# Kernel tuning notes

Measured on AMD Instinct MI355X. Metric: run time of the kernel, lower is better.

Reference implementation:

```python
import jax, jax.numpy as jnp
import numpy as np

B = 64
LMAX = 1024
LENS = np.where(np.arange(B) % 2 == 0, 512, 1024)  # total 49152 residues
NP = int(LENS.sum())
NC_PER = 40
NC = B * NC_PER
DEG_C = 4
DEG_P = 8


def setup_inputs() -> dict:
    key = jax.random.key(0)
    ks = jax.random.split(key, 40)
    rng = np.random.default_rng(0)

    # ragged packing gather: row i of padded conv output contributes its first LENS[i] rows
    prot_gather = jnp.asarray(
        np.concatenate([i * LMAX + np.arange(l) for i, l in enumerate(LENS)]), jnp.int32)
    protein_batch = jnp.asarray(np.repeat(np.arange(B), LENS), jnp.int32)
    compound_batch = jnp.asarray(np.repeat(np.arange(B), NC_PER), jnp.int32)

    # protein edges: within-graph random contacts, DEG_P per residue
    p_starts = np.concatenate([[0], np.cumsum(LENS)])[:-1]
    src, tgt = [], []
    for i, l in enumerate(LENS):
        e = DEG_P * int(l)
        src.append(p_starts[i] + rng.integers(0, l, e))
        tgt.append(p_starts[i] + rng.integers(0, l, e))
    prot_src = jnp.asarray(np.concatenate(src), jnp.int32)
    prot_tgt = jnp.asarray(np.concatenate(tgt), jnp.int32)

    # compound edges: within-graph, DEG_C per atom
    gc = np.repeat(np.arange(B), NC_PER * DEG_C) * NC_PER
    comp_src = jnp.asarray(gc + rng.integers(0, NC_PER, B * NC_PER * DEG_C), jnp.int32)
    comp_tgt = jnp.asarray(gc + rng.integers(0, NC_PER, B * NC_PER * DEG_C), jnp.int32)

    n = lambda k, s: jax.random.normal(ks[k], s, jnp.float32) * 0.05
    return {
        'seq_x': jax.random.normal(ks[0], (B, LMAX, 21), jnp.float32),
        'compound_x': jax.random.normal(ks[1], (NC, 78), jnp.float32),
        'conv_w': n(2, (128, 21, 5)), 'conv_b': n(3, (128,)),
        'c1_wl': n(4, (78, 128)), 'c1_bl': n(5, (128,)), 'c1_wr': n(6, (78, 128)),
        'c2_wl': n(7, (128, 256)), 'c2_bl': n(8, (256,)), 'c2_wr': n(9, (128, 256)),
        'c3_wl': n(10, (256, 512)), 'c3_bl': n(11, (512,)), 'c3_wr': n(12, (256, 512)),
        'cfc_w': n(13, (512, 128)), 'cfc_b': n(14, (128,)),
        'p1_wl': n(15, (128, 128)), 'p1_bl': n(16, (128,)), 'p1_wr': n(17, (128, 128)),
        'p2_wl': n(18, (128, 256)), 'p2_bl': n(19, (256,)), 'p2_wr': n(20, (128, 256)),
        'p3_wl': n(21, (256, 512)), 'p3_bl': n(22, (512,)), 'p3_wr': n(23, (256, 512)),
        'pfc_w': n(24, (512, 128)), 'pfc_b': n(25, (128,)),
        'fc1_w': n(26, (256, 256)), 'fc1_b': n(27, (256,)),
        'out_w': n(28, (256, 1)), 'out_b': n(29, (1,)),
        'prot_gather': prot_gather, 'prot_src': prot_src, 'prot_tgt': prot_tgt,
        'comp_src': comp_src, 'comp_tgt': comp_tgt,
        'protein_batch': protein_batch, 'compound_batch': compound_batch,
    }


def _conv1d(x, w, b):
    # x: [B, L, Cin]; Conv1d(21->128, k=5, stride=1, pad=2)
    y = jax.lax.conv_general_dilated(x.transpose(0, 2, 1), w, (1,), [(2, 2)],
                                     dimension_numbers=('NCH', 'OIH', 'NCH'))
    return y.transpose(0, 2, 1) + b


def _sage(x, src, tgt, wl, bl, wr, n_nodes):
    # PyG SAGEConv(aggr='sum'): lin_l(sum_{j->i} x_j) + lin_r(x_i), lin_r has no bias
    agg = jax.ops.segment_sum(x[src], tgt, num_segments=n_nodes)
    return agg @ wl + bl + x @ wr


def reference(seq_x, compound_x, conv_w, conv_b,
              c1_wl, c1_bl, c1_wr, c2_wl, c2_bl, c2_wr, c3_wl, c3_bl, c3_wr,
              cfc_w, cfc_b,
              p1_wl, p1_bl, p1_wr, p2_wl, p2_bl, p2_wr, p3_wl, p3_bl, p3_wr,
              pfc_w, pfc_b, fc1_w, fc1_b, out_w, out_b,
              prot_gather, prot_src, prot_tgt, comp_src, comp_tgt,
              protein_batch, compound_batch):
    lrelu = jax.nn.leaky_relu  # slope 0.01 == nn.LeakyReLU default
    seq = _conv1d(seq_x, conv_w, conv_b)                 # [B, LMAX, 128]
    p = seq.reshape(-1, seq.shape[-1])[prot_gather]      # ragged pack -> [NP, 128]

    c = compound_x
    c = lrelu(_sage(c, comp_src, comp_tgt, c1_wl, c1_bl, c1_wr, NC))
    c = lrelu(_sage(c, comp_src, comp_tgt, c2_wl, c2_bl, c2_wr, NC))
    c = lrelu(_sage(c, comp_src, comp_tgt, c3_wl, c3_bl, c3_wr, NC))

    p = lrelu(_sage(p, prot_src, prot_tgt, p1_wl, p1_bl, p1_wr, NP))
    p = lrelu(_sage(p, prot_src, prot_tgt, p2_wl, p2_bl, p2_wr, NP))
    p = lrelu(_sage(p, prot_src, prot_tgt, p3_wl, p3_bl, p3_wr, NP))

    c = jax.ops.segment_max(c, compound_batch, num_segments=B)  # global max pool
    c = lrelu(c @ cfc_w + cfc_b)                                # dropout = identity (eval)
    p = jax.ops.segment_max(p, protein_batch, num_segments=B)
    p = lrelu(p @ pfc_w + pfc_b)

    x = jnp.concatenate([c, p], axis=1)
    x = lrelu(x @ fc1_w + fc1_b)
    return x @ out_w + out_b                                    # [B, 1]
```

## Files before the change

### kernel.cpp

```cpp
#include <hip/hip_runtime.h>
#include <hip/hip_fp16.h>

#define B_GRAPHS 64
#define LMAX 1024
#define NP_TOT 49152
#define NC_TOT 2560
#define EP_TOT 393216
#define EC_TOT 10240

#define SCAN_N   (NP_TOT + NC_TOT)
#define SCAN_BLK 512
#define SCAN_NB  (SCAN_N / SCAN_BLK)

typedef _Float16 f16x8 __attribute__((ext_vector_type(8)));
typedef _Float16 f16x4 __attribute__((ext_vector_type(4)));
typedef _Float16 f16x2 __attribute__((ext_vector_type(2)));
typedef float    f32x4 __attribute__((ext_vector_type(4)));

__device__ __forceinline__ float lrelu(float x) { return x > 0.f ? x : 0.01f * x; }

__global__ void zero_int_kernel(int* p, int n) {
    int i = blockIdx.x * blockDim.x + threadIdx.x;
    if (i < n) p[i] = 0;
}

__global__ void hist2_kernel(const int* __restrict__ ptgt, int* __restrict__ pdeg,
                             const int* __restrict__ ctgt, int* __restrict__ cdeg) {
    int e = blockIdx.x * blockDim.x + threadIdx.x;
    if (e < EP_TOT) atomicAdd(&pdeg[ptgt[e]], 1);
    else if (e < EP_TOT + EC_TOT) atomicAdd(&cdeg[ctgt[e - EP_TOT]], 1);
}

__global__ __launch_bounds__(256) void scan_bsum_kernel(
    const int* __restrict__ deg, int* __restrict__ bsums)
{
    __shared__ int red[256];
    int b = blockIdx.x, t = threadIdx.x;
    int2 e = *(const int2*)(deg + b * SCAN_BLK + t * 2);
    red[t] = e.x + e.y;
    __syncthreads();
    for (int s = 128; s > 0; s >>= 1) {
        if (t < s) red[t] += red[t + s];
        __syncthreads();
    }
    if (t == 0) bsums[b] = red[0];
}

__global__ __launch_bounds__(128) void scan_sums_kernel(int* __restrict__ bsums)
{
    __shared__ int v[SCAN_NB];
    int t = threadIdx.x;
    if (t < SCAN_NB) v[t] = bsums[t];
    __syncthreads();
    if (t == 0) {
        int run = 0;
        for (int i = 0; i < SCAN_NB; ++i) { int x = v[i]; v[i] = run; run += x; }
    }
    __syncthreads();
    if (t < SCAN_NB) bsums[t] = v[t];
}

__global__ __launch_bounds__(256) void scan_final_kernel(
    const int* __restrict__ deg, const int* __restrict__ bsums,
    int* __restrict__ p_rowptr, int* __restrict__ c_rowptr)
{
    __shared__ int wsum[4];
    int b = blockIdx.x, t = threadIdx.x;
    int i = b * SCAN_BLK + t * 2;
    int2 e = *(const int2*)(deg + i);
    int ts = e.x + e.y;
    int lane = t & 63, wv = t >> 6;
    int x = ts;
    #pragma unroll
    for (int o = 1; o < 64; o <<= 1) {
        int y = __shfl_up(x, o);
        if (lane >= o) x += y;
    }
    if (lane == 63) wsum[wv] = x;
    __syncthreads();
    int base = bsums[b];
    for (int w = 0; w < wv; ++w) base += wsum[w];
    int excl = base + x - ts;
    int v0 = excl, v1 = excl + e.x;
    if (i < NP_TOT) p_rowptr[i] = v0; else c_rowptr[i - NP_TOT] = v0 - EP_TOT;
    if (i + 1 < NP_TOT) p_rowptr[i + 1] = v1; else c_rowptr[i + 1 - NP_TOT] = v1 - EP_TOT;
    if (b == 0 && t == 0) { p_rowptr[NP_TOT] = EP_TOT; c_rowptr[NC_TOT] = EC_TOT; }
}

__global__ void scatter2_kernel(const int* __restrict__ ps, const int* __restrict__ pt,
                                const int* __restrict__ prow, int* __restrict__ pcur,
                                int* __restrict__ pcsr,
                                const int* __restrict__ cs, const int* __restrict__ ct,
                                const int* __restrict__ crow, int* __restrict__ ccur,
                                int* __restrict__ ccsr) {
    int e = blockIdx.x * blockDim.x + threadIdx.x;
    if (e < EP_TOT) {
        int t = pt[e];
        int pos = atomicAdd(&pcur[t], 1);
        pcsr[prow[t] + pos] = ps[e];
    } else if (e < EP_TOT + EC_TOT) {
        int e2 = e - EP_TOT;
        int t = ct[e2];
        int pos = atomicAdd(&ccur[t], 1);
        ccsr[crow[t] + pos] = cs[e2];
    }
}

struct WJob { const float* in; _Float16* out; int K, D, Kp, mode; };
struct WJobs { WJob j[13]; };

__global__ __launch_bounds__(256) void wprep_all_kernel(WJobs jobs) {
    WJob jb = jobs.j[blockIdx.z];
    int idx = blockIdx.x * 256 + threadIdx.x;
    int total = jb.D * jb.Kp;
    if (idx >= total) return;
    float v;
    if (jb.mode == 0) {
        int d = idx / jb.Kp, k = idx - d * jb.Kp;
        v = (k < jb.K) ? jb.in[(long)k * jb.D + d] : 0.f;
    } else {
        int o = idx >> 7, j = idx & 127;
        if (j < 105) {
            int k = j / 21, c = j - k * 21;
            v = jb.in[o * 105 + c * 5 + k];
        } else v = 0.f;
    }
    jb.out[idx] = (_Float16)v;
}

__global__ void cx_conv_kernel(const float* __restrict__ in, _Float16* __restrict__ out) {
    int i = blockIdx.x * 256 + threadIdx.x;
    if (i >= NC_TOT * 128) return;
    int r = i >> 7, k = i & 127;
    out[i] = (_Float16)(k < 78 ? in[r * 78 + k] : 0.f);
}

__global__ __launch_bounds__(256) void im2col_kernel(
    const float* __restrict__ seq, const int* __restrict__ gather,
    _Float16* __restrict__ out)
{
    int t4 = blockIdx.x * 256 + threadIdx.x;
    int i = t4 >> 5;
    if (i >= NP_TOT) return;
    int j0 = (t4 & 31) * 4;
    int g = gather[i];
    int bb = g >> 10, l = g & (LMAX - 1);
    f16x4 o;
    #pragma unroll
    for (int u = 0; u < 4; ++u) {
        int j = j0 + u;
        float v = 0.f;
        if (j < 105) {
            int k = j / 21, c = j - k * 21;
            int ll = l + k - 2;
            if ((unsigned)ll < (unsigned)LMAX)
                v = seq[((long)bb * LMAX + ll) * 21 + c];
        }
        o[u] = (_Float16)v;
    }
    *(f16x4*)(out + (long)i * 128 + j0) = o;
}

__global__ __launch_bounds__(256) void gemm_f16_kernel(
    const _Float16* __restrict__ A0, const _Float16* __restrict__ WT0,
    const _Float16* __restrict__ A1, const _Float16* __restrict__ WT1,
    const float* __restrict__ bias, _Float16* __restrict__ Out,
    int N, int K, int D, int npass, int act)
{
    __shared__ _Float16 Asm[128 * 64];
    __shared__ _Float16 Bsm[128 * 64];
    const int tid = threadIdx.x;
    const int wave = tid >> 6, lane = tid & 63;
    const int wr = wave >> 1, wc = wave & 1;
    const int l15 = lane & 15, lk = lane >> 4;
    const long r0 = (long)blockIdx.x * 128;
    const long c0 = (long)blockIdx.y * 128;

    const int srow = tid >> 1, shalf = tid & 1;
    int wofs[4];
    #pragma unroll
    for (int j = 0; j < 4; ++j) {
        int c = shalf * 4 + j;
        wofs[j] = srow * 64 + ((c ^ (srow & 7)) * 8);
    }

    int aoff[4][2], boff[4][2];
    #pragma unroll
    for (int m = 0; m < 4; ++m) {
        int row = wr * 64 + m * 16 + l15;
        int col = wc * 64 + m * 16 + l15;
        #pragma unroll
        for (int kk = 0; kk < 2; ++kk) {
            aoff[m][kk] = row * 64 + (((kk * 4 + lk) ^ (row & 7)) * 8);
            boff[m][kk] = col * 64 + (((kk * 4 + lk) ^ (col & 7)) * 8);
        }
    }

    f32x4 acc[4][4];
    #pragma unroll
    for (int m = 0; m < 4; ++m)
        #pragma unroll
        for (int n = 0; n < 4; ++n)
            #pragma unroll
            for (int i = 0; i < 4; ++i) acc[m][n][i] = 0.f;

    const int ksteps = K >> 6;
    const int S = ksteps * npass;

    f16x8 av[4], bv[4];
    #pragma unroll
    for (int j = 0; j < 4; ++j) {
        long kb = (long)(shalf * 4 + j) * 8;
        av[j] = *(const f16x8*)(A0  + (r0 + srow) * K + kb);
        bv[j] = *(const f16x8*)(WT0 + (c0 + srow) * K + kb);
    }

    for (int s = 0; s < S; ++s) {
        __syncthreads();
        #pragma unroll
        for (int j = 0; j < 4; ++j) *(f16x8*)(Asm + wofs[j]) = av[j];
        #pragma unroll
        for (int j = 0; j < 4; ++j) *(f16x8*)(Bsm + wofs[j]) = bv[j];
        __syncthreads();
        if (s + 1 < S) {
            int s1 = s + 1;
            int pass = (s1 >= ksteps) ? 1 : 0;
            long kb0 = (long)(s1 - pass * ksteps) * 64;
            const _Float16* Ax = pass ? A1 : A0;
            const _Float16* Wx = pass ? WT1 : WT0;
            #pragma unroll
            for (int j = 0; j < 4; ++j) {
                long kb = kb0 + (shalf * 4 + j) * 8;
                av[j] = *(const f16x8*)(Ax + (r0 + srow) * K + kb);
                bv[j] = *(const f16x8*)(Wx + (c0 + srow) * K + kb);
            }
        }
        #pragma unroll
        for (int kk = 0; kk < 2; ++kk) {
            f16x8 af[4], bf[4];
            #pragma unroll
            for (int m = 0; m < 4; ++m) af[m] = *(const f16x8*)(Asm + aoff[m][kk]);
            #pragma unroll
            for (int n = 0; n < 4; ++n) bf[n] = *(const f16x8*)(Bsm + boff[n][kk]);
            #pragma unroll
            for (int m = 0; m < 4; ++m)
                #pragma unroll
                for (int n = 0; n < 4; ++n)
                    acc[m][n] = __builtin_amdgcn_mfma_f32_16x16x32_f16(af[m], bf[n], acc[m][n], 0, 0, 0);
        }
    }

    float bn[4]; int coln[4];
    #pragma unroll
    for (int n = 0; n < 4; ++n) {
        coln[n] = (int)c0 + wc * 64 + n * 16 + l15;
        bn[n] = bias[coln[n]];
    }
    #pragma unroll
    for (int m = 0; m < 4; ++m) {
        long rowb = r0 + wr * 64 + m * 16 + lk * 4;
        #pragma unroll
        for (int i = 0; i < 4; ++i) {
            long row = rowb + i;
            #pragma unroll
            for (int n = 0; n < 4; ++n) {
                float v = acc[m][n][i] + bn[n];
                if (act) v = v > 0.f ? v : 0.01f * v;
                Out[row * D + coln[n]] = (_Float16)v;
            }
        }
    }
}

template<int D>
__global__ __launch_bounds__(256) void agg_f16x8_kernel(
    const _Float16* __restrict__ x, const int* __restrict__ rowptr,
    const int* __restrict__ csr, _Float16* __restrict__ agg, int n)
{
    constexpr int LPN = D / 8;
    int node = (blockIdx.x * 256 + threadIdx.x) / LPN;
    int lane = threadIdx.x & (LPN - 1);
    if (node >= n) return;
    int beg = rowptr[node], end = rowptr[node + 1];
    float acc[8] = {};
    const long lo = lane * 8;
    for (int j = beg; j < end; j += 4) {
        int r = end - j;
        int s0 = csr[j];
        int s1 = (r > 1) ? csr[j + 1] : s0;
        int s2 = (r > 2) ? csr[j + 2] : s0;
        int s3 = (r > 3) ? csr[j + 3] : s0;
        f16x8 v0 = *(const f16x8*)(x + (long)s0 * D + lo);
        f16x8 v1 = *(const f16x8*)(x + (long)s1 * D + lo);
        f16x8 v2 = *(const f16x8*)(x + (long)s2 * D + lo);
        f16x8 v3 = *(const f16x8*)(x + (long)s3 * D + lo);
        #pragma unroll
        for (int u = 0; u < 8; ++u) acc[u] += (float)v0[u];
        if (r > 1) {
            #pragma unroll
            for (int u = 0; u < 8; ++u) acc[u] += (float)v1[u];
        }
        if (r > 2) {
            #pragma unroll
            for (int u = 0; u < 8; ++u) acc[u] += (float)v2[u];
        }
        if (r > 3) {
            #pragma unroll
            for (int u = 0; u < 8; ++u) acc[u] += (float)v3[u];
        }
    }
    f16x8 o;
    #pragma unroll
    for (int u = 0; u < 8; ++u) o[u] = (_Float16)acc[u];
    *(f16x8*)(agg + (long)node * D + lo) = o;
}

__global__ __launch_bounds__(256) void pool_comp_kernel(
    const _Float16* __restrict__ x, float* __restrict__ out)
{
    __shared__ float sm[4][512];
    int g = blockIdx.x;
    int cg = threadIdx.x & 63, rs = threadIdx.x >> 6;
    float m[8];
    #pragma unroll
    for (int u = 0; u < 8; ++u) m[u] = -INFINITY;
    for (int r = rs; r < 40; r += 4) {
        f16x8 v = *(const f16x8*)(x + (long)(g * 40 + r) * 512 + cg * 8);
        #pragma unroll
        for (int u = 0; u < 8; ++u) m[u] = fmaxf(m[u], (float)v[u]);
    }
    #pragma unroll
    for (int u = 0; u < 8; ++u) sm[rs][cg * 8 + u] = m[u];
    __syncthreads();
    if (rs == 0) {
        #pragma unroll
        for (int u = 0; u < 8; ++u) {
            int c = cg * 8 + u;
            out[g * 512 + c] = fmaxf(fmaxf(sm[0][c], sm[1][c]), fmaxf(sm[2][c], sm[3][c]));
        }
    }
}

#define PSPLIT 8
#define PPART  (PSPLIT * 4)
__global__ __launch_bounds__(256) void pool_prot_partial_kernel(
    const _Float16* __restrict__ x, float* __restrict__ part)
{
    int g = blockIdx.x, s = blockIdx.y;
    int cg = threadIdx.x & 63, rs = threadIdx.x >> 6;
    int start = 512 * ((g + 1) / 2) + 1024 * (g / 2);
    int len = (g & 1) ? 1024 : 512;
    int chunk = len / PSPLIT;
    int sub = chunk >> 2;
    long r0 = start + s * chunk + rs * sub;
    float m[8];
    #pragma unroll
    for (int u = 0; u < 8; ++u) m[u] = -INFINITY;
    for (int r = 0; r < sub; ++r) {
        f16x8 v = *(const f16x8*)(x + (r0 + r) * 512 + cg * 8);
        #pragma unroll
        for (int u = 0; u < 8; ++u) m[u] = fmaxf(m[u], (float)v[u]);
    }
    float* o = part + (long)((g * PSPLIT + s) * 4 + rs) * 512 + cg * 8;
    #pragma unroll
    for (int u = 0; u < 8; ++u) o[u] = m[u];
}

__global__ __launch_bounds__(256) void pool_prot_final_kernel(
    const float* __restrict__ part, float* __restrict__ out)
{
    int g = blockIdx.x;
    int col = blockIdx.y * 256 + threadIdx.x;
    float m = -INFINITY;
    #pragma unroll 8
    for (int p = 0; p < PPART; ++p)
        m = fmaxf(m, part[(long)(g * PPART + p) * 512 + col]);
    out[g * 512 + col] = m;
}

__global__ __launch_bounds__(256) void head_kernel(
    const float* __restrict__ cpool, const float* __restrict__ ppool,
    const float* __restrict__ cfc_w, const float* __restrict__ cfc_b,
    const float* __restrict__ pfc_w, const float* __restrict__ pfc_b,
    const float* __restrict__ fc1_w, const float* __restrict__ fc1_b,
    const float* __restrict__ out_w, const float* __restrict__ out_b,
    float* __restrict__ out)
{
    __shared__ float cp[512], pp[512], cf[128], pf[128], h[256], red[256];
    int g = blockIdx.x, t = threadIdx.x;
    for (int i = t; i < 512; i += 256) {
        cp[i] = cpool[g * 512 + i];
        pp[i] = ppool[g * 512 + i];
    }
    __syncthreads();
    if (t < 128) {
        float a = cfc_b[t];
        for (int k = 0; k < 512; k++) a += cp[k] * cfc_w[k * 128 + t];
        cf[t] = lrelu(a);
    } else {
        int o = t - 128;
        float a = pfc_b[o];
        for (int k = 0; k < 512; k++) a += pp[k] * pfc_w[k * 128 + o];
        pf[o] = lrelu(a);
    }
    __syncthreads();
    {
        float a = fc1_b[t];
        for (int k = 0; k < 128; k++) a += cf[k] * fc1_w[k * 256 + t];
        for (int k = 0; k < 128; k++) a += pf[k] * fc1_w[(128 + k) * 256 + t];
        h[t] = lrelu(a);
    }
    __syncthreads();
    red[t] = h[t] * out_w[t];
    __syncthreads();
    for (int s = 128; s > 0; s >>= 1) {
        if (t < s) red[t] += red[t + s];
        __syncthreads();
    }
    if (t == 0) out[g] = red[0] + out_b[0];
}

extern "C" void kernel_launch(void* const* d_in, const int* in_sizes, int n_in,
                              void* d_out, int out_size, void* d_ws, size_t ws_size,
                              hipStream_t stream) {
    const float* seq_x      = (const float*)d_in[0];
    const float* compound_x = (const float*)d_in[1];
    const float* conv_w     = (const float*)d_in[2];
    const float* conv_b     = (const float*)d_in[3];
    const float* c1_wl = (const float*)d_in[4];
    const float* c1_bl = (const float*)d_in[5];
    const float* c1_wr = (const float*)d_in[6];
    const float* c2_wl = (const float*)d_in[7];
    const float* c2_bl = (const float*)d_in[8];
    const float* c2_wr = (const float*)d_in[9];
    const float* c3_wl = (const float*)d_in[10];
    const float* c3_bl = (const float*)d_in[11];
    const float* c3_wr = (const float*)d_in[12];
    const float* cfc_w = (const float*)d_in[13];
    const float* cfc_b = (const float*)d_in[14];
    const float* p1_wl = (const float*)d_in[15];
    const float* p1_bl = (const float*)d_in[16];
    const float* p1_wr = (const float*)d_in[17];
    const float* p2_wl = (const float*)d_in[18];
    const float* p2_bl = (const float*)d_in[19];
    const float* p2_wr = (const float*)d_in[20];
    const float* p3_wl = (const float*)d_in[21];
    const float* p3_bl = (const float*)d_in[22];
    const float* p3_wr = (const float*)d_in[23];
    const float* pfc_w = (const float*)d_in[24];
    const float* pfc_b = (const float*)d_in[25];
    const float* fc1_w = (const float*)d_in[26];
    const float* fc1_b = (const float*)d_in[27];
    const float* out_w = (const float*)d_in[28];
    const float* out_b = (const float*)d_in[29];
    const int* prot_gather = (const int*)d_in[30];
    const int* prot_src    = (const int*)d_in[31];
    const int* prot_tgt    = (const int*)d_in[32];
    const int* comp_src    = (const int*)d_in[33];
    const int* comp_tgt    = (const int*)d_in[34];

    float* out = (float*)d_out;

    size_t off = 0;
    auto alloc = [&](size_t bytes) -> char* {
        char* p = (char*)d_ws + off;
        off = (off + bytes + 255) & ~(size_t)255;
        return p;
    };
    _Float16* pim   = (_Float16*)alloc((size_t)NP_TOT * 128 * 2);
    _Float16* pconv = (_Float16*)alloc((size_t)NP_TOT * 128 * 2);
    _Float16* pagg  = (_Float16*)alloc((size_t)NP_TOT * 256 * 2);
    _Float16* pl1   = (_Float16*)alloc((size_t)NP_TOT * 128 * 2);
    _Float16* pl2   = (_Float16*)alloc((size_t)NP_TOT * 256 * 2);
    _Float16* pl3   = (_Float16*)alloc((size_t)NP_TOT * 512 * 2);
    _Float16* cxp   = (_Float16*)alloc((size_t)NC_TOT * 128 * 2);
    _Float16* cagg  = (_Float16*)alloc((size_t)NC_TOT * 256 * 2);
    _Float16* cl1   = (_Float16*)alloc((size_t)NC_TOT * 128 * 2);
    _Float16* cl2   = (_Float16*)alloc((size_t)NC_TOT * 256 * 2);
    _Float16* cl3   = (_Float16*)alloc((size_t)NC_TOT * 512 * 2);
    _Float16* wt_p1l = (_Float16*)alloc(128 * 128 * 2);
    _Float16* wt_p1r = (_Float16*)alloc(128 * 128 * 2);
    _Float16* wt_p2l = (_Float16*)alloc(256 * 128 * 2);
    _Float16* wt_p2r = (_Float16*)alloc(256 * 128 * 2);
    _Float16* wt_p3l = (_Float16*)alloc(512 * 256 * 2);
    _Float16* wt_p3r = (_Float16*)alloc(512 * 256 * 2);
    _Float16* wt_c1l = (_Float16*)alloc(128 * 128 * 2);
    _Float16* wt_c1r = (_Float16*)alloc(128 * 128 * 2);
    _Float16* wt_c2l = (_Float16*)alloc(256 * 128 * 2);
    _Float16* wt_c2r = (_Float16*)alloc(256 * 128 * 2);
    _Float16* wt_c3l = (_Float16*)alloc(512 * 256 * 2);
    _Float16* wt_c3r = (_Float16*)alloc(512 * 256 * 2);
    _Float16* wt_cv  = (_Float16*)alloc(128 * 128 * 2);
    float* cpool = (float*)alloc(B_GRAPHS * 512 * 4);
    float* ppool = (float*)alloc(B_GRAPHS * 512 * 4);
    float* ppart = (float*)alloc((size_t)B_GRAPHS * PPART * 512 * 4);
    int* cursors  = (int*)alloc((NP_TOT + NC_TOT) * 4);
    int* p_cursor = cursors;
    int* c_cursor = cursors + NP_TOT;
    int* p_rowptr = (int*)alloc((NP_TOT + 1) * 4);
    int* p_csr    = (int*)alloc(EP_TOT * 4);
    int* c_rowptr = (int*)alloc((NC_TOT + 1) * 4);
    int* c_csr    = (int*)alloc(EC_TOT * 4);
    int* bsums    = (int*)alloc(SCAN_NB * 4);
    (void)ws_size; (void)n_in; (void)in_sizes; (void)out_size;

    WJobs jobs;
    jobs.j[0]  = { p1_wl, wt_p1l, 128, 128, 128, 0 };
    jobs.j[1]  = { p1_wr, wt_p1r, 128, 128, 128, 0 };
    jobs.j[2]  = { p2_wl, wt_p2l, 128, 256, 128, 0 };
    jobs.j[3]  = { p2_wr, wt_p2r, 128, 256, 128, 0 };
    jobs.j[4]  = { p3_wl, wt_p3l, 256, 512, 256, 0 };
    jobs.j[5]  = { p3_wr, wt_p3r, 256, 512, 256, 0 };
    jobs.j[6]  = { c1_wl, wt_c1l,  78, 128, 128, 0 };
    jobs.j[7]  = { c1_wr, wt_c1r,  78, 128, 128, 0 };
    jobs.j[8]  = { c2_wl, wt_c2l, 128, 256, 128, 0 };
    jobs.j[9]  = { c2_wr, wt_c2r, 128, 256, 128, 0 };
    jobs.j[10] = { c3_wl, wt_c3l, 256, 512, 256, 0 };
    jobs.j[11] = { c3_wr, wt_c3r, 256, 512, 256, 0 };
    jobs.j[12] = { conv_w, wt_cv, 105, 128, 128, 1 };
    wprep_all_kernel<<<dim3(512, 1, 13), 256, 0, stream>>>(jobs);
    cx_conv_kernel<<<(NC_TOT * 128 + 255) / 256, 256, 0, stream>>>(compound_x, cxp);

    zero_int_kernel<<<(SCAN_N + 255) / 256, 256, 0, stream>>>(cursors, SCAN_N);
    hist2_kernel<<<(EP_TOT + EC_TOT + 255) / 256, 256, 0, stream>>>(prot_tgt, p_cursor, comp_tgt, c_cursor);
    scan_bsum_kernel<<<SCAN_NB, 256, 0, stream>>>(cursors, bsums);
    scan_sums_kernel<<<1, 128, 0, stream>>>(bsums);
    scan_final_kernel<<<SCAN_NB, 256, 0, stream>>>(cursors, bsums, p_rowptr, c_rowptr);
    zero_int_kernel<<<(SCAN_N + 255) / 256, 256, 0, stream>>>(cursors, SCAN_N);
    scatter2_kernel<<<(EP_TOT + EC_TOT + 255) / 256, 256, 0, stream>>>(
        prot_src, prot_tgt, p_rowptr, p_cursor, p_csr,
        comp_src, comp_tgt, c_rowptr, c_cursor, c_csr);

    im2col_kernel<<<(NP_TOT * 32 + 255) / 256, 256, 0, stream>>>(seq_x, prot_gather, pim);
    gemm_f16_kernel<<<dim3(NP_TOT / 128, 1), 256, 0, stream>>>(
        pim, wt_cv, pim, wt_cv, conv_b, pconv, NP_TOT, 128, 128, 1, 0);

    agg_f16x8_kernel<128><<<(NC_TOT * 16 + 255) / 256, 256, 0, stream>>>(cxp, c_rowptr, c_csr, cagg, NC_TOT);
    gemm_f16_kernel<<<dim3(NC_TOT / 128, 1), 256, 0, stream>>>(
        cagg, wt_c1l, cxp, wt_c1r, c1_bl, cl1, NC_TOT, 128, 128, 2, 1);
    agg_f16x8_kernel<128><<<(NC_TOT * 16 + 255) / 256, 256, 0, stream>>>(cl1, c_rowptr, c_csr, cagg, NC_TOT);
    gemm_f16_kernel<<<dim3(NC_TOT / 128, 2), 256, 0, stream>>>(
        cagg, wt_c2l, cl1, wt_c2r, c2_bl, cl2, NC_TOT, 128, 256, 2, 1);
    agg_f16x8_kernel<256><<<(NC_TOT * 32 + 255) / 256, 256, 0, stream>>>(cl2, c_rowptr, c_csr, cagg, NC_TOT);
    gemm_f16_kernel<<<dim3(NC_TOT / 128, 4), 256, 0, stream>>>(
        cagg, wt_c3l, cl2, wt_c3r, c3_bl, cl3, NC_TOT, 256, 512, 2, 1);
    pool_comp_kernel<<<B_GRAPHS, 256, 0, stream>>>(cl3, cpool);

    agg_f16x8_kernel<128><<<(NP_TOT * 16 + 255) / 256, 256, 0, stream>>>(pconv, p_rowptr, p_csr, pagg, NP_TOT);
    gemm_f16_kernel<<<dim3(NP_TOT / 128, 1), 256, 0, stream>>>(
        pagg, wt_p1l, pconv, wt_p1r, p1_bl, pl1, NP_TOT, 128, 128, 2, 1);
    agg_f16x8_kernel<128><<<(NP_TOT * 16 + 255) / 256, 256, 0, stream>>>(pl1, p_rowptr, p_csr, pagg, NP_TOT);
    gemm_f16_kernel<<<dim3(NP_TOT / 128, 2), 256, 0, stream>>>(
        pagg, wt_p2l, pl1, wt_p2r, p2_bl, pl2, NP_TOT, 128, 256, 2, 1);
    agg_f16x8_kernel<256><<<(NP_TOT * 32 + 255) / 256, 256, 0, stream>>>(pl2, p_rowptr, p_csr, pagg, NP_TOT);
    gemm_f16_kernel<<<dim3(NP_TOT / 128, 4), 256, 0, stream>>>(
        pagg, wt_p3l, pl2, wt_p3r, p3_bl, pl3, NP_TOT, 256, 512, 2, 1);
    pool_prot_partial_kernel<<<dim3(B_GRAPHS, PSPLIT), 256, 0, stream>>>(pl3, ppart);
    pool_prot_final_kernel<<<dim3(B_GRAPHS, 2), 256, 0, stream>>>(ppart, ppool);

    head_kernel<<<B_GRAPHS, 256, 0, stream>>>(cpool, ppool, cfc_w, cfc_b, pfc_w, pfc_b,
                                              fc1_w, fc1_b, out_w, out_b, out);
}
```

Baseline: 400.5 us.

## Double-buffer GEMM LDS tiles and remap blocks for XCD-aware locality

The GEMM kernel now keeps two LDS buffers for the A and B tiles. It stores the next tile while computing on the current one and prefetches two steps ahead, so each k-step needs one barrier instead of two. Launches switch to a 1D grid, and each block index is remapped so that consecutive tiles land on the same XCD, with row and column tiles taken from the flat index. This is meant to cut barrier stalls and improve L2 reuse of A rows across column tiles. The cost is doubled LDS (64KB) and more registers, which may reduce occupancy.

```diff
diff --git a/kernel.cpp b/kernel.cpp
--- a/kernel.cpp
+++ b/kernel.cpp
@@ -167,14 +167,22 @@
     const float* __restrict__ bias, _Float16* __restrict__ Out,
     int N, int K, int D, int npass, int act)
 {
-    __shared__ _Float16 Asm[128 * 64];
-    __shared__ _Float16 Bsm[128 * 64];
+    __shared__ _Float16 Asm[2][128 * 64];
+    __shared__ _Float16 Bsm[2][128 * 64];
     const int tid = threadIdx.x;
     const int wave = tid >> 6, lane = tid & 63;
     const int wr = wave >> 1, wc = wave & 1;
     const int l15 = lane & 15, lk = lane >> 4;
-    const long r0 = (long)blockIdx.x * 128;
-    const long c0 = (long)blockIdx.y * 128;
+
+    const int nwg = gridDim.x;
+    const int bid = blockIdx.x;
+    const int q = nwg >> 3, r8 = nwg & 7;
+    const int xcd = bid & 7, sl = bid >> 3;
+    const int wg = (xcd < r8) ? (xcd * (q + 1) + sl)
+                              : (r8 * (q + 1) + (xcd - r8) * q + sl);
+    const int DC = D >> 7;
+    const long r0 = (long)(wg / DC) * 128;
+    const long c0 = (long)(wg % DC) * 128;
 
     const int srow = tid >> 1, shalf = tid & 1;
     int wofs[4];
@@ -207,47 +215,55 @@
     const int ksteps = K >> 6;
     const int S = ksteps * npass;
 
-    f16x8 av[4], bv[4];
+    f16x8 ha[4], hb[4];
+    auto LOADT = [&](int st) {
+        int pass = (st >= ksteps) ? 1 : 0;
+        long kb0 = (long)(st - pass * ksteps) * 64;
+        const _Float16* Ax = pass ? A1 : A0;
+        const _Float16* Wx = pass ? WT1 : WT0;
+        #pragma unroll
+        for (int j = 0; j < 4; ++j) {
+            long kb = kb0 + (shalf * 4 + j) * 8;
+            ha[j] = *(const f16x8*)(Ax + (r0 + srow) * K + kb);
+            hb[j] = *(const f16x8*)(Wx + (c0 + srow) * K + kb);
+        }
+    };
+
+    LOADT(0);
     #pragma unroll
     for (int j = 0; j < 4; ++j) {
-        long kb = (long)(shalf * 4 + j) * 8;
-        av[j] = *(const f16x8*)(A0  + (r0 + srow) * K + kb);
-        bv[j] = *(const f16x8*)(WT0 + (c0 + srow) * K + kb);
-    }
+        *(f16x8*)(&Asm[0][0] + wofs[j]) = ha[j];
+        *(f16x8*)(&Bsm[0][0] + wofs[j]) = hb[j];
+    }
+    if (S > 1) LOADT(1);
+    __syncthreads();
 
     for (int s = 0; s < S; ++s) {
-        __syncthreads();
-        #pragma unroll
-        for (int j = 0; j < 4; ++j) *(f16x8*)(Asm + wofs[j]) = av[j];
-        #pragma unroll
-        for (int j = 0; j < 4; ++j) *(f16x8*)(Bsm + wofs[j]) = bv[j];
-        __syncthreads();
+        int cur = s & 1, nxt = cur ^ 1;
         if (s + 1 < S) {
-            int s1 = s + 1;
-            int pass = (s1 >= ksteps) ? 1 : 0;
-            long kb0 = (long)(s1 - pass * ksteps) * 64;
-            const _Float16* Ax = pass ? A1 : A0;
-            const _Float16* Wx = pass ? WT1 : WT0;
             #pragma unroll
             for (int j = 0; j < 4; ++j) {
-                long kb = kb0 + (shalf * 4 + j) * 8;
-                av[j] = *(const f16x8*)(Ax + (r0 + srow) * K + kb);
-                bv[j] = *(const f16x8*)(Wx + (c0 + srow) * K + kb);
+                *(f16x8*)(&Asm[nxt][0] + wofs[j]) = ha[j];
+                *(f16x8*)(&Bsm[nxt][0] + wofs[j]) = hb[j];
             }
         }
+        if (s + 2 < S) LOADT(s + 2);
+        const _Float16* As = &Asm[cur][0];
+        const _Float16* Bs = &Bsm[cur][0];
         #pragma unroll
         for (int kk = 0; kk < 2; ++kk) {
             f16x8 af[4], bf[4];
             #pragma unroll
-            for (int m = 0; m < 4; ++m) af[m] = *(const f16x8*)(Asm + aoff[m][kk]);
-            #pragma unroll
-            for (int n = 0; n < 4; ++n) bf[n] = *(const f16x8*)(Bsm + boff[n][kk]);
+            for (int m = 0; m < 4; ++m) af[m] = *(const f16x8*)(As + aoff[m][kk]);
+            #pragma unroll
+            for (int n = 0; n < 4; ++n) bf[n] = *(const f16x8*)(Bs + boff[n][kk]);
             #pragma unroll
             for (int m = 0; m < 4; ++m)
                 #pragma unroll
                 for (int n = 0; n < 4; ++n)
                     acc[m][n] = __builtin_amdgcn_mfma_f32_16x16x32_f16(af[m], bf[n], acc[m][n], 0, 0, 0);
         }
+        __syncthreads();
     }
 
     float bn[4]; int coln[4];
@@ -532,28 +548,28 @@
         comp_src, comp_tgt, c_rowptr, c_cursor, c_csr);
 
     im2col_kernel<<<(NP_TOT * 32 + 255) / 256, 256, 0, stream>>>(seq_x, prot_gather, pim);
-    gemm_f16_kernel<<<dim3(NP_TOT / 128, 1), 256, 0, stream>>>(
+    gemm_f16_kernel<<<NP_TOT / 128, 256, 0, stream>>>(
         pim, wt_cv, pim, wt_cv, conv_b, pconv, NP_TOT, 128, 128, 1, 0);
 
     agg_f16x8_kernel<128><<<(NC_TOT * 16 + 255) / 256, 256, 0, stream>>>(cxp, c_rowptr, c_csr, cagg, NC_TOT);
-    gemm_f16_kernel<<<dim3(NC_TOT / 128, 1), 256, 0, stream>>>(
+    gemm_f16_kernel<<<NC_TOT / 128, 256, 0, stream>>>(
         cagg, wt_c1l, cxp, wt_c1r, c1_bl, cl1, NC_TOT, 128, 128, 2, 1);
     agg_f16x8_kernel<128><<<(NC_TOT * 16 + 255) / 256, 256, 0, stream>>>(cl1, c_rowptr, c_csr, cagg, NC_TOT);
-    gemm_f16_kernel<<<dim3(NC_TOT / 128, 2), 256, 0, stream>>>(
+    gemm_f16_kernel<<<(NC_TOT / 128) * 2, 256, 0, stream>>>(
         cagg, wt_c2l, cl1, wt_c2r, c2_bl, cl2, NC_TOT, 128, 256, 2, 1);
     agg_f16x8_kernel<256><<<(NC_TOT * 32 + 255) / 256, 256, 0, stream>>>(cl2, c_rowptr, c_csr, cagg, NC_TOT);
-    gemm_f16_kernel<<<dim3(NC_TOT / 128, 4), 256, 0, stream>>>(
+    gemm_f16_kernel<<<(NC_TOT / 128) * 4, 256, 0, stream>>>(
         cagg, wt_c3l, cl2, wt_c3r, c3_bl, cl3, NC_TOT, 256, 512, 2, 1);
     pool_comp_kernel<<<B_GRAPHS, 256, 0, stream>>>(cl3, cpool);
 
     agg_f16x8_kernel<128><<<(NP_TOT * 16 + 255) / 256, 256, 0, stream>>>(pconv, p_rowptr, p_csr, pagg, NP_TOT);
-    gemm_f16_kernel<<<dim3(NP_TOT / 128, 1), 256, 0, stream>>>(
+    gemm_f16_kernel<<<NP_TOT / 128, 256, 0, stream>>>(
         pagg, wt_p1l, pconv, wt_p1r, p1_bl, pl1, NP_TOT, 128, 128, 2, 1);
     agg_f16x8_kernel<128><<<(NP_TOT * 16 + 255) / 256, 256, 0, stream>>>(pl1, p_rowptr, p_csr, pagg, NP_TOT);
-    gemm_f16_kernel<<<dim3(NP_TOT / 128, 2), 256, 0, stream>>>(
+    gemm_f16_kernel<<<(NP_TOT / 128) * 2, 256, 0, stream>>>(
         pagg, wt_p2l, pl1, wt_p2r, p2_bl, pl2, NP_TOT, 128, 256, 2, 1);
     agg_f16x8_kernel<256><<<(NP_TOT * 32 + 255) / 256, 256, 0, stream>>>(pl2, p_rowptr, p_csr, pagg, NP_TOT);
-    gemm_f16_kernel<<<dim3(NP_TOT / 128, 4), 256, 0, stream>>>(
+    gemm_f16_kernel<<<(NP_TOT / 128) * 4, 256, 0, stream>>>(
         pagg, wt_p3l, pl2, wt_p3r, p3_bl, pl3, NP_TOT, 256, 512, 2, 1);
     pool_prot_partial_kernel<<<dim3(B_GRAPHS, PSPLIT), 256, 0, stream>>>(pl3, ppart);
     pool_prot_final_kernel<<<dim3(B_GRAPHS, 2), 256, 0, stream>>>(ppart, ppool);
```

New measurement: 405.5 us. About the same (+1.3%).

## Batch protein and compound SAGE layers into shared launches with XCD-aware tile mapping

Applied to the files above, without the earlier changes.

Each aggregation and GEMM launch now carries two job descriptors, so the protein and compound branches for the same layer run in one grid instead of separate kernels. This removes six launches and lets the small compound work fill idle CUs alongside the protein work. The GEMM block index is also remapped so consecutive tiles land on the same XCD, and the row and column tile are derived from a flattened index, which is meant to improve L2 reuse of A rows across column tiles. The cost is a little extra per-block index arithmetic and job selection.

```diff
diff --git a/kernel.cpp b/kernel.cpp
--- a/kernel.cpp
+++ b/kernel.cpp
@@ -161,11 +161,14 @@
     *(f16x4*)(out + (long)i * 128 + j0) = o;
 }
 
-__global__ __launch_bounds__(256) void gemm_f16_kernel(
-    const _Float16* __restrict__ A0, const _Float16* __restrict__ WT0,
-    const _Float16* __restrict__ A1, const _Float16* __restrict__ WT1,
-    const float* __restrict__ bias, _Float16* __restrict__ Out,
-    int N, int K, int D, int npass, int act)
+struct GemmJob {
+    const _Float16* A0; const _Float16* WT0;
+    const _Float16* A1; const _Float16* WT1;
+    const float* bias; _Float16* Out;
+    int N, K, D, npass, act, nwg;
+};
+
+__global__ __launch_bounds__(256) void gemm_f16_kernel(GemmJob jp, GemmJob jc)
 {
     __shared__ _Float16 Asm[128 * 64];
     __shared__ _Float16 Bsm[128 * 64];
@@ -173,15 +176,27 @@
     const int wave = tid >> 6, lane = tid & 63;
     const int wr = wave >> 1, wc = wave & 1;
     const int l15 = lane & 15, lk = lane >> 4;
-    const long r0 = (long)blockIdx.x * 128;
-    const long c0 = (long)blockIdx.y * 128;
+
+    const int bid = blockIdx.x;
+    const GemmJob& j = (bid < jp.nwg) ? jp : jc;
+    const int lb = (bid < jp.nwg) ? bid : bid - jp.nwg;
+    const int K = j.K, D = j.D;
+
+    const int nwg = j.nwg;
+    const int q = nwg >> 3, r8 = nwg & 7;
+    const int xcd = lb & 7, sl = lb >> 3;
+    const int wg = (xcd < r8) ? (xcd * (q + 1) + sl)
+                              : (r8 * (q + 1) + (xcd - r8) * q + sl);
+    const int DC = D >> 7;
+    const long r0 = (long)(wg / DC) * 128;
+    const long c0 = (long)(wg % DC) * 128;
 
     const int srow = tid >> 1, shalf = tid & 1;
     int wofs[4];
     #pragma unroll
-    for (int j = 0; j < 4; ++j) {
-        int c = shalf * 4 + j;
-        wofs[j] = srow * 64 + ((c ^ (srow & 7)) * 8);
+    for (int jj = 0; jj < 4; ++jj) {
+        int c = shalf * 4 + jj;
+        wofs[jj] = srow * 64 + ((c ^ (srow & 7)) * 8);
     }
 
     int aoff[4][2], boff[4][2];
@@ -205,34 +220,34 @@
             for (int i = 0; i < 4; ++i) acc[m][n][i] = 0.f;
 
     const int ksteps = K >> 6;
-    const int S = ksteps * npass;
+    const int S = ksteps * j.npass;
 
     f16x8 av[4], bv[4];
     #pragma unroll
-    for (int j = 0; j < 4; ++j) {
-        long kb = (long)(shalf * 4 + j) * 8;
-        av[j] = *(const f16x8*)(A0  + (r0 + srow) * K + kb);
-        bv[j] = *(const f16x8*)(WT0 + (c0 + srow) * K + kb);
+    for (int jj = 0; jj < 4; ++jj) {
+        long kb = (long)(shalf * 4 + jj) * 8;
+        av[jj] = *(const f16x8*)(j.A0  + (r0 + srow) * K + kb);
+        bv[jj] = *(const f16x8*)(j.WT0 + (c0 + srow) * K + kb);
     }
 
     for (int s = 0; s < S; ++s) {
         __syncthreads();
         #pragma unroll
-        for (int j = 0; j < 4; ++j) *(f16x8*)(Asm + wofs[j]) = av[j];
-        #pragma unroll
-        for (int j = 0; j < 4; ++j) *(f16x8*)(Bsm + wofs[j]) = bv[j];
+        for (int jj = 0; jj < 4; ++jj) *(f16x8*)(Asm + wofs[jj]) = av[jj];
+        #pragma unroll
+        for (int jj = 0; jj < 4; ++jj) *(f16x8*)(Bsm + wofs[jj]) = bv[jj];
         __syncthreads();
         if (s + 1 < S) {
             int s1 = s + 1;
             int pass = (s1 >= ksteps) ? 1 : 0;
             long kb0 = (long)(s1 - pass * ksteps) * 64;
-            const _Float16* Ax = pass ? A1 : A0;
-            const _Float16* Wx = pass ? WT1 : WT0;
-            #pragma unroll
-            for (int j = 0; j < 4; ++j) {
-                long kb = kb0 + (shalf * 4 + j) * 8;
-                av[j] = *(const f16x8*)(Ax + (r0 + srow) * K + kb);
-                bv[j] = *(const f16x8*)(Wx + (c0 + srow) * K + kb);
+            const _Float16* Ax = pass ? j.A1 : j.A0;
+            const _Float16* Wx = pass ? j.WT1 : j.WT0;
+            #pragma unroll
+            for (int jj = 0; jj < 4; ++jj) {
+                long kb = kb0 + (shalf * 4 + jj) * 8;
+                av[jj] = *(const f16x8*)(Ax + (r0 + srow) * K + kb);
+                bv[jj] = *(const f16x8*)(Wx + (c0 + srow) * K + kb);
             }
         }
         #pragma unroll
@@ -254,7 +269,7 @@
     #pragma unroll
     for (int n = 0; n < 4; ++n) {
         coln[n] = (int)c0 + wc * 64 + n * 16 + l15;
-        bn[n] = bias[coln[n]];
+        bn[n] = j.bias[coln[n]];
     }
     #pragma unroll
     for (int m = 0; m < 4; ++m) {
@@ -265,31 +280,39 @@
             #pragma unroll
             for (int n = 0; n < 4; ++n) {
                 float v = acc[m][n][i] + bn[n];
-                if (act) v = v > 0.f ? v : 0.01f * v;
-                Out[row * D + coln[n]] = (_Float16)v;
+                if (j.act) v = v > 0.f ? v : 0.01f * v;
+                j.Out[row * D + coln[n]] = (_Float16)v;
             }
         }
     }
 }
 
+struct AggJob {
+    const _Float16* x; const int* rowptr; const int* csr;
+    _Float16* agg; int n, nwg;
+};
+
 template<int D>
-__global__ __launch_bounds__(256) void agg_f16x8_kernel(
-    const _Float16* __restrict__ x, const int* __restrict__ rowptr,
-    const int* __restrict__ csr, _Float16* __restrict__ agg, int n)
+__global__ __launch_bounds__(256) void agg_f16x8_kernel(AggJob ja, AggJob jb)
 {
     constexpr int LPN = D / 8;
-    int node = (blockIdx.x * 256 + threadIdx.x) / LPN;
+    int bid = blockIdx.x;
+    const AggJob& j = (bid < ja.nwg) ? ja : jb;
+    int lb = (bid < ja.nwg) ? bid : bid - ja.nwg;
+    int node = (lb * 256 + threadIdx.x) / LPN;
     int lane = threadIdx.x & (LPN - 1);
-    if (node >= n) return;
-    int beg = rowptr[node], end = rowptr[node + 1];
+    if (node >= j.n) return;
+    int beg = j.rowptr[node], end = j.rowptr[node + 1];
     float acc[8] = {};
     const long lo = lane * 8;
-    for (int j = beg; j < end; j += 4) {
-        int r = end - j;
-        int s0 = csr[j];
-        int s1 = (r > 1) ? csr[j + 1] : s0;
-        int s2 = (r > 2) ? csr[j + 2] : s0;
-        int s3 = (r > 3) ? csr[j + 3] : s0;
+    const _Float16* x = j.x;
+    const int* csr = j.csr;
+    for (int jj = beg; jj < end; jj += 4) {
+        int r = end - jj;
+        int s0 = csr[jj];
+        int s1 = (r > 1) ? csr[jj + 1] : s0;
+        int s2 = (r > 2) ? csr[jj + 2] : s0;
+        int s3 = (r > 3) ? csr[jj + 3] : s0;
         f16x8 v0 = *(const f16x8*)(x + (long)s0 * D + lo);
         f16x8 v1 = *(const f16x8*)(x + (long)s1 * D + lo);
         f16x8 v2 = *(const f16x8*)(x + (long)s2 * D + lo);
@@ -312,7 +335,7 @@
     f16x8 o;
     #pragma unroll
     for (int u = 0; u < 8; ++u) o[u] = (_Float16)acc[u];
-    *(f16x8*)(agg + (long)node * D + lo) = o;
+    *(f16x8*)(j.agg + (long)node * D + lo) = o;
 }
 
 __global__ __launch_bounds__(256) void pool_comp_kernel(
@@ -532,29 +555,38 @@
         comp_src, comp_tgt, c_rowptr, c_cursor, c_csr);
 
     im2col_kernel<<<(NP_TOT * 32 + 255) / 256, 256, 0, stream>>>(seq_x, prot_gather, pim);
-    gemm_f16_kernel<<<dim3(NP_TOT / 128, 1), 256, 0, stream>>>(
-        pim, wt_cv, pim, wt_cv, conv_b, pconv, NP_TOT, 128, 128, 1, 0);
-
-    agg_f16x8_kernel<128><<<(NC_TOT * 16 + 255) / 256, 256, 0, stream>>>(cxp, c_rowptr, c_csr, cagg, NC_TOT);
-    gemm_f16_kernel<<<dim3(NC_TOT / 128, 1), 256, 0, stream>>>(
-        cagg, wt_c1l, cxp, wt_c1r, c1_bl, cl1, NC_TOT, 128, 128, 2, 1);
-    agg_f16x8_kernel<128><<<(NC_TOT * 16 + 255) / 256, 256, 0, stream>>>(cl1, c_rowptr, c_csr, cagg, NC_TOT);
-    gemm_f16_kernel<<<dim3(NC_TOT / 128, 2), 256, 0, stream>>>(
-        cagg, wt_c2l, cl1, wt_c2r, c2_bl, cl2, NC_TOT, 128, 256, 2, 1);
-    agg_f16x8_kernel<256><<<(NC_TOT * 32 + 255) / 256, 256, 0, stream>>>(cl2, c_rowptr, c_csr, cagg, NC_TOT);
-    gemm_f16_kernel<<<dim3(NC_TOT / 128, 4), 256, 0, stream>>>(
-        cagg, wt_c3l, cl2, wt_c3r, c3_bl, cl3, NC_TOT, 256, 512, 2, 1);
+    {
+        GemmJob jp = { pim, wt_cv, pim, wt_cv, conv_b, pconv, NP_TOT, 128, 128, 1, 0, NP_TOT / 128 };
+        GemmJob jc = jp; jc.nwg = 0;
+        gemm_f16_kernel<<<jp.nwg, 256, 0, stream>>>(jp, jc);
+    }
+
+    {
+        AggJob ap = { pconv, p_rowptr, p_csr, pagg, NP_TOT, (NP_TOT * 16 + 255) / 256 };
+        AggJob ac = { cxp,   c_rowptr, c_csr, cagg, NC_TOT, (NC_TOT * 16 + 255) / 256 };
+        agg_f16x8_kernel<128><<<ap.nwg + ac.nwg, 256, 0, stream>>>(ap, ac);
+        GemmJob jp = { pagg, wt_p1l, pconv, wt_p1r, p1_bl, pl1, NP_TOT, 128, 128, 2, 1, NP_TOT / 128 };
+        GemmJob jc = { cagg, wt_c1l, cxp,   wt_c1r, c1_bl, cl1, NC_TOT, 128, 128, 2, 1, NC_TOT / 128 };
+        gemm_f16_kernel<<<jp.nwg + jc.nwg, 256, 0, stream>>>(jp, jc);
+    }
+    {
+        AggJob ap = { pl1, p_rowptr, p_csr, pagg, NP_TOT, (NP_TOT * 16 + 255) / 256 };
+        AggJob ac = { cl1, c_rowptr, c_csr, cagg, NC_TOT, (NC_TOT * 16 + 255) / 256 };
+        agg_f16x8_kernel<128><<<ap.nwg + ac.nwg, 256, 0, stream>>>(ap, ac);
+        GemmJob jp = { pagg, wt_p2l, pl1, wt_p2r, p2_bl, pl2, NP_TOT, 128, 256, 2, 1, (NP_TOT / 128) * 2 };
+        GemmJob jc = { cagg, wt_c2l, cl1, wt_c2r, c2_bl, cl2, NC_TOT, 128, 256, 2, 1, (NC_TOT / 128) * 2 };
+        gemm_f16_kernel<<<jp.nwg + jc.nwg, 256, 0, stream>>>(jp, jc);
+    }
+    {
+        AggJob ap = { pl2, p_rowptr, p_csr, pagg, NP_TOT, (NP_TOT * 32 + 255) / 256 };
+        AggJob ac = { cl2, c_rowptr, c_csr, cagg, NC_TOT, (NC_TOT * 32 + 255) / 256 };
+        agg_f16x8_kernel<256><<<ap.nwg + ac.nwg, 256, 0, stream>>>(ap, ac);
+        GemmJob jp = { pagg, wt_p3l, pl2, wt_p3r, p3_bl, pl3, NP_TOT, 256, 512, 2, 1, (NP_TOT / 128) * 4 };
+        GemmJob jc = { cagg, wt_c3l, cl2, wt_c3r, c3_bl, cl3, NC_TOT, 256, 512, 2, 1, (NC_TOT / 128) * 4 };
+        gemm_f16_kernel<<<jp.nwg + jc.nwg, 256, 0, stream>>>(jp, jc);
+    }
+
     pool_comp_kernel<<<B_GRAPHS, 256, 0, stream>>>(cl3, cpool);
-
-    agg_f16x8_kernel<128><<<(NP_TOT * 16 + 255) / 256, 256, 0, stream>>>(pconv, p_rowptr, p_csr, pagg, NP_TOT);
-    gemm_f16_kernel<<<dim3(NP_TOT / 128, 1), 256, 0, stream>>>(
-        pagg, wt_p1l, pconv, wt_p1r, p1_bl, pl1, NP_TOT, 128, 128, 2, 1);
-    agg_f16x8_kernel<128><<<(NP_TOT * 16 + 255) / 256, 256, 0, stream>>>(pl1, p_rowptr, p_csr, pagg, NP_TOT);
-    gemm_f16_kernel<<<dim3(NP_TOT / 128, 2), 256, 0, stream>>>(
-        pagg, wt_p2l, pl1, wt_p2r, p2_bl, pl2, NP_TOT, 128, 256, 2, 1);
-    agg_f16x8_kernel<256><<<(NP_TOT * 32 + 255) / 256, 256, 0, stream>>>(pl2, p_rowptr, p_csr, pagg, NP_TOT);
-    gemm_f16_kernel<<<dim3(NP_TOT / 128, 4), 256, 0, stream>>>(
-        pagg, wt_p3l, pl2, wt_p3r, p3_bl, pl3, NP_TOT, 256, 512, 2, 1);
     pool_prot_partial_kernel<<<dim3(B_GRAPHS, PSPLIT), 256, 0, stream>>>(pl3, ppart);
     pool_prot_final_kernel<<<dim3(B_GRAPHS, 2), 256, 0, stream>>>(ppart, ppool);
 
```

New measurement: 367.2 us. -8.3%, faster.
